# Kernel tuning notes

Hardware: AMD Instinct MI355X
Metric: run time of the kernel (lower is better)

Reference implementation:

```python
import jax, jax.numpy as jnp
import numpy as np

T = 32          # chain length (init arg)
K = 2048        # particles per timestep (Ks)
RES = 0.5       # observed scalar (init buffer)
LIKE_STD = 1.0  # likelihood std (init arg)
LOG2PI = float(np.log(2.0 * np.pi))


def _logpdf(x, mu, std):
    # Normal(mu, std).log_prob(x)
    z = (x - mu) / std
    return -0.5 * z * z - jnp.log(std) - 0.5 * LOG2PI


def logmmmeanexp(X, Y):
    # log( exp(X) @ exp(Y) / X.shape[1] ), numerically stabilized exactly as the torch code
    x = jnp.max(X, axis=1, keepdims=True)
    y = jnp.max(Y, axis=0, keepdims=True)
    return x + y + jnp.log(jnp.exp(X - x) @ jnp.exp(Y - y)) - jnp.log(jnp.asarray(X.shape[1], X.dtype))


def setup_inputs() -> dict:
    key = jax.random.key(0)
    eps = jax.random.normal(key, (T, K), dtype=jnp.float32)
    means = jnp.zeros((T,), jnp.float32)
    # matches the torch init: sqrt((1+arange(T))/T)
    log_stds = jnp.sqrt((1.0 + jnp.arange(T, dtype=jnp.float32)) / T)
    return {"means": means, "log_stds": log_stds, "eps": eps}


def reference(means, log_stds, eps):
    std = jnp.exp(log_stds)                            # proposal stds, (T,)
    zs = means[:, None] + std[:, None] * eps           # reparameterized samples, (T,K)
    log_q = _logpdf(zs, means[:, None], std[:, None])  # proposal log-probs, (T,K)
    sp = jnp.sqrt(1.0 / T)                             # prior/transition std

    # first factor: prior over z_0 minus proposal, (1,K)
    r0 = (_logpdf(zs[0], 0.0, sp) - log_q[0])[None, :]
    # middle factors: transition log-probs, (T-1, K, K); Ms[i][j,k] = logN(zs[i+1,k]; zs[i,j], sp) - log_q[i+1,k]
    Ms = _logpdf(zs[1:, None, :], zs[:-1, :, None], sp) - log_q[1:, None, :]

    def step(r, M):
        return logmmmeanexp(r, M), None

    r, _ = jax.lax.scan(step, r0, Ms)
    # likelihood factor, (K,1)
    L = _logpdf(jnp.float32(RES), zs[-1][:, None], jnp.float32(LIKE_STD))
    return logmmmeanexp(r, L)  # (1,1) log marginal-likelihood estimate
```

## Files before the change

### kernel.cpp

```cpp
#include <hip/hip_runtime.h>
#include <math.h>

#define T 32
#define K 2048
#define NBLOCKS 256
#define NTHREADS 512
#define HB 128
#define CPB 16
#define QS 4
#define SSTRIDE 32
#define L2E_F 1.4426950408889634f
#define LN2_F 0.6931471805599453f
#define LOG2PI_F 1.8378770664093453f
#define SP_F     0.17677669529663687f
#define LOG_SP_F (-1.7328679513998633f)
#define CNORM_F  (-(LOG_SP_F) - 0.5f * LOG2PI_F)

#if __has_builtin(__builtin_amdgcn_exp2f)
#define EXP2F(x) __builtin_amdgcn_exp2f(x)
#else
#define EXP2F(x) exp2f(x)
#endif
#if __has_builtin(__builtin_amdgcn_logf)
#define LOG2F(x) __builtin_amdgcn_logf(x)
#else
#define LOG2F(x) log2f(x)
#endif

__device__ __forceinline__ float aload4(const float* p) {
    return __hip_atomic_load(p, __ATOMIC_RELAXED, __HIP_MEMORY_SCOPE_AGENT);
}
__device__ __forceinline__ void astore4(float* p, float v) {
    __hip_atomic_store(p, v, __ATOMIC_RELAXED, __HIP_MEMORY_SCOPE_AGENT);
}
__device__ __forceinline__ int sload(const int* p) {
    return __hip_atomic_load(p, __ATOMIC_RELAXED, __HIP_MEMORY_SCOPE_AGENT);
}
__device__ __forceinline__ void sstore(int* p, int v) {
    __hip_atomic_store(p, v, __ATOMIC_RELAXED, __HIP_MEMORY_SCOPE_AGENT);
}

__global__ __launch_bounds__(NTHREADS) void fused_kernel(
    const float* __restrict__ means, const float* __restrict__ log_stds,
    const float* __restrict__ eps, float* __restrict__ fbuf,
    float* __restrict__ bbuf, int* __restrict__ fsent, int* __restrict__ bsent,
    float* __restrict__ out)
{
    __shared__ float2 shzD[2][K];
    __shared__ float2 lzc[T][CPB];
    __shared__ float smu[T], sstd[T], slq2[T];
    __shared__ float red[NTHREADS];
    __shared__ int ldsflag;

    const int tid  = threadIdx.x;
    const int b    = blockIdx.x;
    const bool fwd = (b < HB);
    const int lb   = fwd ? b : b - HB;
    const int col0 = lb * CPB;

    if (tid == 0) ldsflag = 0;

    {
        int t = tid >> 4, dcol = tid & 15;
        float mu = means[t];
        float st = expf(log_stds[t]);
        if (dcol == 0) {
            smu[t] = mu; sstd[t] = st;
            slq2[t] = L2E_F * (logf(st) + 0.5f * LOG2PI_F);
        }
        float e = eps[t * K + col0 + dcol];
        float z = fmaf(st, e, mu);
        float log_q = fmaf(-0.5f * e, e, -logf(st) - 0.5f * LOG2PI_F);
        float tz2 = (32.0f * L2E_F) * z;
        if (fwd) {
            float cm2 = fmaf((-16.0f * L2E_F) * z, z,
                             L2E_F * (CNORM_F - log_q)) - 11.0f;
            lzc[t][dcol] = make_float2(tz2, cm2);
            if (t == 0) {
                float r0 = fmaf(-16.0f * z, z, CNORM_F) - log_q;
                astore4(&fbuf[col0 + dcol], r0 * L2E_F);
            }
        } else {
            float cm2 = fmaf((-16.0f * L2E_F) * z, z, L2E_F * CNORM_F) - 11.0f;
            lzc[t][dcol] = make_float2(tz2, cm2);
            if (t == T - 1) {
                float d = 0.5f - z;
                float c31 = fmaf(-0.5f * d, d, -0.5f * LOG2PI_F);
                astore4(&bbuf[col0 + dcol], c31 * L2E_F);
            }
        }
    }
    __syncthreads();
    int* mysent = fwd ? fsent : bsent;
    if (tid == 0) sstore(&mysent[lb * SSTRIDE], 1);

    const int lane = tid & 63;
    const int wave = tid >> 6;
    float* mybuf = fwd ? fbuf : bbuf;
    const int nstep = fwd ? 16 : 15;

    for (int p = 0; p < nstep; ++p) {
        const int par  = p & 1;
        const int need = p + 1;
        const int tin  = fwd ? p : 31 - p;
        const int town = fwd ? p + 1 : 30 - p;
        const float mu_i  = smu[tin];
        const float std_i = sstd[tin];
        const float lqc   = slq2[tin];
        const float* erow = eps + tin * K;

        float zloc[QS], dadd[QS];
        #pragma unroll
        for (int q = 0; q < QS; ++q) {
            float e = erow[tid + q * NTHREADS];
            float z = fmaf(std_i, e, mu_i);
            zloc[q] = z;
            float base = fwd ? 0.0f : fmaf((0.5f * L2E_F) * e, e, lqc);
            dadd[q] = fmaf((-16.0f * L2E_F) * z, z, base);
        }

        if (wave == 0) {
            const int* s0 = mysent + lane * SSTRIDE;
            const int* s1 = mysent + (lane + 64) * SSTRIDE;
            for (;;) {
                int v0 = sload(s0);
                int v1 = sload(s1);
                if (__all(min(v0, v1) >= need)) break;
                __builtin_amdgcn_s_sleep(1);
            }
            __hip_atomic_store(&ldsflag, need, __ATOMIC_RELEASE,
                               __HIP_MEMORY_SCOPE_WORKGROUP);
        } else {
            while (__hip_atomic_load(&ldsflag, __ATOMIC_ACQUIRE,
                                     __HIP_MEMORY_SCOPE_WORKGROUP) < need)
                __builtin_amdgcn_s_sleep(1);
        }

        const float* mrow = mybuf + par * K;
        float rv[QS];
        #pragma unroll
        for (int q = 0; q < QS; ++q) rv[q] = aload4(&mrow[tid + q * NTHREADS]);
        #pragma unroll
        for (int q = 0; q < QS; ++q)
            shzD[par][tid + q * NTHREADS] = make_float2(zloc[q], rv[q] + dadd[q]);
        __syncthreads();

        const float4* shp = (const float4*)&shzD[par][0];
        float2 zcA = lzc[town][2 * wave];
        float2 zcB = lzc[town][2 * wave + 1];
        float4 fr[16];
        #pragma unroll
        for (int i = 0; i < 16; ++i) fr[i] = shp[lane + (i << 6)];
        float m0 = -INFINITY, m1 = -INFINITY;
        #pragma unroll
        for (int i = 0; i < 16; ++i) {
            m0 = fmaxf(m0, fmaxf(fmaf(zcA.x, fr[i].x, fr[i].y),
                                 fmaf(zcA.x, fr[i].z, fr[i].w)));
            m1 = fmaxf(m1, fmaxf(fmaf(zcB.x, fr[i].x, fr[i].y),
                                 fmaf(zcB.x, fr[i].z, fr[i].w)));
        }
        #pragma unroll
        for (int off = 32; off >= 1; off >>= 1) {
            m0 = fmaxf(m0, __shfl_xor(m0, off, 64));
            m1 = fmaxf(m1, __shfl_xor(m1, off, 64));
        }
        float s0 = 0.0f, s1 = 0.0f;
        #pragma unroll
        for (int i = 0; i < 16; ++i) {
            s0 += EXP2F(fmaf(zcA.x, fr[i].x, fr[i].y) - m0);
            s0 += EXP2F(fmaf(zcA.x, fr[i].z, fr[i].w) - m0);
            s1 += EXP2F(fmaf(zcB.x, fr[i].x, fr[i].y) - m1);
            s1 += EXP2F(fmaf(zcB.x, fr[i].z, fr[i].w) - m1);
        }
        #pragma unroll
        for (int off = 32; off >= 1; off >>= 1) {
            s0 += __shfl_xor(s0, off, 64);
            s1 += __shfl_xor(s1, off, 64);
        }
        if (lane < 2) {
            float mm = lane ? m1 : m0;
            float sv = lane ? s1 : s0;
            float cm = lane ? zcB.y : zcA.y;
            astore4(&mybuf[(par ^ 1) * K + col0 + 2 * wave + lane],
                    cm + mm + LOG2F(sv));
        }
        __syncthreads();
        if (tid == 0) sstore(&mysent[lb * SSTRIDE], p + 2);
    }

    if (b == 0) {
        for (;;) {
            int f0 = sload(&fsent[lane * SSTRIDE]);
            int f1 = sload(&fsent[(lane + 64) * SSTRIDE]);
            int g0 = sload(&bsent[lane * SSTRIDE]);
            int g1 = sload(&bsent[(lane + 64) * SSTRIDE]);
            bool ok = (min(f0, f1) >= 17) && (min(g0, g1) >= 16);
            if (__all(ok)) break;
            __builtin_amdgcn_s_sleep(1);
        }
        float vals[QS];
        float m = -INFINITY;
        #pragma unroll
        for (int q = 0; q < QS; ++q) {
            int j = tid + q * NTHREADS;
            float v = aload4(&fbuf[j]) + aload4(&bbuf[K + j]);
            vals[q] = v;
            m = fmaxf(m, v);
        }
        red[tid] = m; __syncthreads();
        for (int off = NTHREADS / 2; off >= 1; off >>= 1) {
            if (tid < off) red[tid] = fmaxf(red[tid], red[tid + off]);
            __syncthreads();
        }
        m = red[0]; __syncthreads();
        float ssum = 0.0f;
        #pragma unroll
        for (int q = 0; q < QS; ++q) ssum += EXP2F(vals[q] - m);
        red[tid] = ssum; __syncthreads();
        for (int off = NTHREADS / 2; off >= 1; off >>= 1) {
            if (tid < off) red[tid] += red[tid + off];
            __syncthreads();
        }
        if (tid == 0) out[0] = LN2_F * (m + LOG2F(red[0]) - 11.0f);
    }
}

extern "C" void kernel_launch(void* const* d_in, const int* in_sizes, int n_in,
                              void* d_out, int out_size, void* d_ws, size_t ws_size,
                              hipStream_t stream) {
    const float* means    = (const float*)d_in[0];
    const float* log_stds = (const float*)d_in[1];
    const float* eps      = (const float*)d_in[2];
    float* out = (float*)d_out;

    float* fbuf = (float*)d_ws;
    float* bbuf = fbuf + 2 * K;
    int*   fsent = (int*)(bbuf + 2 * K);
    int*   bsent = fsent + 128 * SSTRIDE;

    fused_kernel<<<NBLOCKS, NTHREADS, 0, stream>>>(
        means, log_stds, eps, fbuf, bbuf, fsent, bsent, out);
}
```

Measured before the change: 113.7 us.

## Tag exchanged values with step counters and prefetch them before the barrier wait

Each value exchanged between blocks is now stored as a 64-bit pair holding the value and the step number, written with a single atomic store. Each block issues its loads of the next row before spinning on the sentinel flags. After the wait, it reloads only the entries whose tag does not match the expected step. The goal is to hide global-memory load latency behind the cross-block synchronisation wait. The cost is double the exchange-buffer traffic and workspace size. There is also a risk: tags left in the workspace from a previous launch can match the expected step, so a stale value could be accepted.

```diff
diff --git a/kernel.cpp b/kernel.cpp
--- a/kernel.cpp
+++ b/kernel.cpp
@@ -27,11 +27,17 @@
 #define LOG2F(x) log2f(x)
 #endif
 
-__device__ __forceinline__ float aload4(const float* p) {
-    return __hip_atomic_load(p, __ATOMIC_RELAXED, __HIP_MEMORY_SCOPE_AGENT);
-}
-__device__ __forceinline__ void astore4(float* p, float v) {
-    __hip_atomic_store(p, v, __ATOMIC_RELAXED, __HIP_MEMORY_SCOPE_AGENT);
+union Pack { float2 f; unsigned long long u; };
+__device__ __forceinline__ float2 aload8(const float2* p) {
+    Pack pk;
+    pk.u = __hip_atomic_load((const unsigned long long*)p,
+                             __ATOMIC_RELAXED, __HIP_MEMORY_SCOPE_AGENT);
+    return pk.f;
+}
+__device__ __forceinline__ void astore8(float2* p, float v, int tag) {
+    Pack pk; pk.f.x = v; pk.f.y = __int_as_float(tag);
+    __hip_atomic_store((unsigned long long*)p, pk.u,
+                       __ATOMIC_RELAXED, __HIP_MEMORY_SCOPE_AGENT);
 }
 __device__ __forceinline__ int sload(const int* p) {
     return __hip_atomic_load(p, __ATOMIC_RELAXED, __HIP_MEMORY_SCOPE_AGENT);
@@ -42,8 +48,8 @@
 
 __global__ __launch_bounds__(NTHREADS) void fused_kernel(
     const float* __restrict__ means, const float* __restrict__ log_stds,
-    const float* __restrict__ eps, float* __restrict__ fbuf,
-    float* __restrict__ bbuf, int* __restrict__ fsent, int* __restrict__ bsent,
+    const float* __restrict__ eps, float2* __restrict__ fbuf,
+    float2* __restrict__ bbuf, int* __restrict__ fsent, int* __restrict__ bsent,
     float* __restrict__ out)
 {
     __shared__ float2 shzD[2][K];
@@ -78,7 +84,7 @@
             lzc[t][dcol] = make_float2(tz2, cm2);
             if (t == 0) {
                 float r0 = fmaf(-16.0f * z, z, CNORM_F) - log_q;
-                astore4(&fbuf[col0 + dcol], r0 * L2E_F);
+                astore8(&fbuf[col0 + dcol], r0 * L2E_F, 1);
             }
         } else {
             float cm2 = fmaf((-16.0f * L2E_F) * z, z, L2E_F * CNORM_F) - 11.0f;
@@ -86,7 +92,7 @@
             if (t == T - 1) {
                 float d = 0.5f - z;
                 float c31 = fmaf(-0.5f * d, d, -0.5f * LOG2PI_F);
-                astore4(&bbuf[col0 + dcol], c31 * L2E_F);
+                astore8(&bbuf[col0 + dcol], c31 * L2E_F, 1);
             }
         }
     }
@@ -96,7 +102,7 @@
 
     const int lane = tid & 63;
     const int wave = tid >> 6;
-    float* mybuf = fwd ? fbuf : bbuf;
+    float2* mybuf = fwd ? fbuf : bbuf;
     const int nstep = fwd ? 16 : 15;
 
     for (int p = 0; p < nstep; ++p) {
@@ -108,6 +114,11 @@
         const float std_i = sstd[tin];
         const float lqc   = slq2[tin];
         const float* erow = eps + tin * K;
+
+        const float2* mrow = mybuf + par * K;
+        float2 rv[QS];
+        #pragma unroll
+        for (int q = 0; q < QS; ++q) rv[q] = aload8(&mrow[tid + q * NTHREADS]);
 
         float zloc[QS], dadd[QS];
         #pragma unroll
@@ -136,13 +147,15 @@
                 __builtin_amdgcn_s_sleep(1);
         }
 
-        const float* mrow = mybuf + par * K;
-        float rv[QS];
-        #pragma unroll
-        for (int q = 0; q < QS; ++q) rv[q] = aload4(&mrow[tid + q * NTHREADS]);
         #pragma unroll
         for (int q = 0; q < QS; ++q)
-            shzD[par][tid + q * NTHREADS] = make_float2(zloc[q], rv[q] + dadd[q]);
+            if (__float_as_int(rv[q].y) != need)
+                rv[q] = aload8(&mrow[tid + q * NTHREADS]);
+
+        #pragma unroll
+        for (int q = 0; q < QS; ++q)
+            shzD[par][tid + q * NTHREADS] =
+                make_float2(zloc[q], rv[q].x + dadd[q]);
         __syncthreads();
 
         const float4* shp = (const float4*)&shzD[par][0];
@@ -181,8 +194,8 @@
             float mm = lane ? m1 : m0;
             float sv = lane ? s1 : s0;
             float cm = lane ? zcB.y : zcA.y;
-            astore4(&mybuf[(par ^ 1) * K + col0 + 2 * wave + lane],
-                    cm + mm + LOG2F(sv));
+            astore8(&mybuf[(par ^ 1) * K + col0 + 2 * wave + lane],
+                    cm + mm + LOG2F(sv), p + 2);
         }
         __syncthreads();
         if (tid == 0) sstore(&mysent[lb * SSTRIDE], p + 2);
@@ -203,7 +216,7 @@
         #pragma unroll
         for (int q = 0; q < QS; ++q) {
             int j = tid + q * NTHREADS;
-            float v = aload4(&fbuf[j]) + aload4(&bbuf[K + j]);
+            float v = aload8(&fbuf[j]).x + aload8(&bbuf[K + j]).x;
             vals[q] = v;
             m = fmaxf(m, v);
         }
@@ -233,8 +246,8 @@
     const float* eps      = (const float*)d_in[2];
     float* out = (float*)d_out;
 
-    float* fbuf = (float*)d_ws;
-    float* bbuf = fbuf + 2 * K;
+    float2* fbuf = (float2*)d_ws;
+    float2* bbuf = fbuf + 2 * K;
     int*   fsent = (int*)(bbuf + 2 * K);
     int*   bsent = fsent + 128 * SSTRIDE;
 
```

Result: slower. 119.2 us (+4.8%).
